# Kernel optimization log

Hardware: AMD Instinct MI355X
Metric: run time of the kernel (lower is better)

The kernel has to match this reference:

```python
import jax, jax.numpy as jnp
import numpy as np

TOPK = 8

def setup_inputs() -> dict:
    key = jax.random.key(0)
    k1, k2, k3, k4, k5 = jax.random.split(key, 5)
    B, S, D, E = 8, 2048, 4096, 64
    scale = 1.0 / np.sqrt(D)
    x = jax.random.normal(k1, (B, S, D), dtype=jnp.float32)
    Wr = jax.random.uniform(k2, (D, E), dtype=jnp.float32, minval=-scale, maxval=scale)
    br = jax.random.uniform(k3, (E,), dtype=jnp.float32, minval=-scale, maxval=scale)
    Wn = jax.random.uniform(k4, (D, E), dtype=jnp.float32, minval=-scale, maxval=scale)
    bn = jax.random.uniform(k5, (E,), dtype=jnp.float32, minval=-scale, maxval=scale)
    return {"x": x, "Wr": Wr, "br": br, "Wn": Wn, "bn": bn}

def reference(x, Wr, br, Wn, bn):
    B, S, D = x.shape
    E = Wr.shape[1]
    logits = jnp.einsum('bsd,de->bse', x, Wr) + br          # [B,S,E]
    # NOTE: original module computes noisy_logits = logits + randn*noisy_vec but
    # then takes topk/softmax on the CLEAN logits, so the noise branch is dead code.
    noisy_vec = jnp.einsum('bsd,de->bse', x, Wn) + bn       # computed, unused (faithful)
    del noisy_vec
    topk_vals, topk_idx = jax.lax.top_k(logits, TOPK)       # [B,S,K]
    T = B * S
    flat_vals = topk_vals.reshape(T, TOPK)
    flat_idx = topk_idx.reshape(T, TOPK)
    sparse = jnp.full((T, E), -jnp.inf, dtype=logits.dtype)
    sparse = sparse.at[jnp.arange(T)[:, None], flat_idx].set(flat_vals)
    router_scores = jax.nn.softmax(sparse, axis=-1).reshape(B, S, E)
    return router_scores, topk_idx
```

## Files before the change

### kernel.cpp

```cpp
#include <hip/hip_runtime.h>
#include <math.h>

#define DDIM 4096
#define EDIM 64
#define NROWS 16384
#define MBLK 32
#define KT 64
#define NKT (DDIM / KT)
#define TOPK_K 8
#define DIGIT_BIAS 0x00808080

typedef int i32x4 __attribute__((ext_vector_type(4)));

__device__ __forceinline__ int digits_of(float f) {
  int v = __float2int_rn(f);
  return (v + DIGIT_BIAS) ^ DIGIT_BIAS;
}

__device__ __forceinline__ unsigned perm_b32(unsigned a, unsigned b, unsigned sel) {
#if __has_builtin(__builtin_amdgcn_perm)
  return __builtin_amdgcn_perm(a, b, sel);
#else
  union { unsigned u[2]; unsigned char c[8]; } s; s.u[0] = b; s.u[1] = a;
  unsigned r = 0;
  for (int i = 0; i < 4; ++i) r |= (unsigned)s.c[(sel >> (8*i)) & 7] << (8*i);
  return r;
#endif
}

__global__ __launch_bounds__(256) void wr_convert(const float* __restrict__ Wr,
                                                  char* __restrict__ wl8) {
  int t = blockIdx.x * 256 + threadIdx.x;
  int e = t & 63, k16 = t >> 6;
  int kt64 = k16 >> 2, kgg = k16 & 3, nf = e >> 4, col = e & 15;
  int D[16];
  #pragma unroll
  for (int j = 0; j < 16; ++j)
    D[j] = digits_of(Wr[(size_t)(k16 * 16 + j) * EDIM + e] * 68719476736.0f);
  #pragma unroll
  for (int pl = 0; pl < 4; ++pl) {
    unsigned wv[4];
    #pragma unroll
    for (int g = 0; g < 4; ++g)
      wv[g] = ((unsigned)((D[4*g+0] >> (8*pl)) & 255))
            | ((unsigned)((D[4*g+1] >> (8*pl)) & 255) << 8)
            | ((unsigned)((D[4*g+2] >> (8*pl)) & 255) << 16)
            | ((unsigned)((D[4*g+3] >> (8*pl)) & 255) << 24);
    i32x4 val = {(int)wv[0], (int)wv[1], (int)wv[2], (int)wv[3]};
    *(i32x4*)(wl8 + (size_t)pl * 262144 + (size_t)(kt64 * 4 + nf) * 1024
              + (size_t)(kgg * 16 + col) * 16) = val;
  }
}

__global__ __launch_bounds__(512, 4) void router_fused(
    const float* __restrict__ x, const char* __restrict__ wl8,
    const float* __restrict__ br,
    float* __restrict__ out_scores, float* __restrict__ out_idx) {
  __shared__ __align__(16) char smem[2][24576];

  const int tid  = threadIdx.x;
  const int lane = tid & 63;
  const int w    = tid >> 6;
  const int mw   = w >> 2;
  const int nw   = w & 3;
  const int kg   = lane >> 4;
  const int row0 = blockIdx.x * MBLK;
  const int row_l = mw * 16 + (lane & 15);
  const int srow = w * 4 + (lane >> 4);
  const float bias = br[nw * 16 + (lane & 15)];

  i32x4 acc[5] = {};

  auto stage = [&](int t, int b) {
    #pragma unroll
    for (int i = 0; i < 2; ++i) {
      int c = w * 2 + i;
      int plane = c >> 2, nf = c & 3;
      const char* src = wl8 + (size_t)plane * 262144 +
                        (size_t)(t * 4 + nf) * 1024 + (size_t)lane * 16;
      __builtin_amdgcn_global_load_lds(
          (const __attribute__((address_space(1))) unsigned int*)(const void*)src,
          (__attribute__((address_space(3))) unsigned int*)(void*)&smem[b][c * 1024],
          16, 0, 0);
    }
    {
      int cc = lane & 15;
      const float* src = x + (size_t)(row0 + srow) * DDIM + t * KT
                           + ((cc ^ (srow & 7)) << 2);
      __builtin_amdgcn_global_load_lds(
          (const __attribute__((address_space(1))) unsigned int*)(const void*)src,
          (__attribute__((address_space(3))) unsigned int*)(void*)
              &smem[b][16384 + w * 1024],
          16, 0, 0);
    }
  };

  auto compute = [&](int b) {
    const char* Wb = smem[b];
    const char* Xb = smem[b] + 16384;
    float4 xv[4];
    #pragma unroll
    for (int c = 0; c < 4; ++c) {
      int chunk = (kg * 4 + c) ^ (row_l & 7);
      xv[c] = *(const float4*)(Xb + row_l * 256 + chunk * 16);
    }
    i32x4 a0, a1, a2, a3;
    #pragma unroll
    for (int g = 0; g < 4; ++g) {
      float4 v = xv[g];
      unsigned f0 = (unsigned)digits_of(v.x * 33554432.0f);
      unsigned f1 = (unsigned)digits_of(v.y * 33554432.0f);
      unsigned f2 = (unsigned)digits_of(v.z * 33554432.0f);
      unsigned f3 = (unsigned)digits_of(v.w * 33554432.0f);
      unsigned zl01 = perm_b32(f1, f0, 0x05010400u);
      unsigned zh01 = perm_b32(f1, f0, 0x07030602u);
      unsigned zl23 = perm_b32(f3, f2, 0x05010400u);
      unsigned zh23 = perm_b32(f3, f2, 0x07030602u);
      a0[g] = (int)perm_b32(zl23, zl01, 0x05040100u);
      a1[g] = (int)perm_b32(zl23, zl01, 0x07060302u);
      a2[g] = (int)perm_b32(zh23, zh01, 0x05040100u);
      a3[g] = (int)perm_b32(zh23, zh01, 0x07060302u);
    }
    i32x4 b0 = *(const i32x4*)(Wb + (0 * 4 + nw) * 1024 + lane * 16);
    i32x4 b1 = *(const i32x4*)(Wb + (1 * 4 + nw) * 1024 + lane * 16);
    i32x4 b2 = *(const i32x4*)(Wb + (2 * 4 + nw) * 1024 + lane * 16);
    i32x4 b3 = *(const i32x4*)(Wb + (3 * 4 + nw) * 1024 + lane * 16);

    acc[0] = __builtin_amdgcn_mfma_i32_16x16x64_i8(a3, b3, acc[0], 0, 0, 0);
    acc[1] = __builtin_amdgcn_mfma_i32_16x16x64_i8(a3, b2, acc[1], 0, 0, 0);
    acc[1] = __builtin_amdgcn_mfma_i32_16x16x64_i8(a2, b3, acc[1], 0, 0, 0);
    acc[2] = __builtin_amdgcn_mfma_i32_16x16x64_i8(a3, b1, acc[2], 0, 0, 0);
    acc[2] = __builtin_amdgcn_mfma_i32_16x16x64_i8(a2, b2, acc[2], 0, 0, 0);
    acc[2] = __builtin_amdgcn_mfma_i32_16x16x64_i8(a1, b3, acc[2], 0, 0, 0);
    acc[3] = __builtin_amdgcn_mfma_i32_16x16x64_i8(a3, b0, acc[3], 0, 0, 0);
    acc[3] = __builtin_amdgcn_mfma_i32_16x16x64_i8(a2, b1, acc[3], 0, 0, 0);
    acc[3] = __builtin_amdgcn_mfma_i32_16x16x64_i8(a1, b2, acc[3], 0, 0, 0);
    acc[3] = __builtin_amdgcn_mfma_i32_16x16x64_i8(a0, b3, acc[3], 0, 0, 0);
    acc[4] = __builtin_amdgcn_mfma_i32_16x16x64_i8(a2, b0, acc[4], 0, 0, 0);
    acc[4] = __builtin_amdgcn_mfma_i32_16x16x64_i8(a1, b1, acc[4], 0, 0, 0);
    acc[4] = __builtin_amdgcn_mfma_i32_16x16x64_i8(a0, b2, acc[4], 0, 0, 0);
  };

  stage(0, 0);
  __syncthreads();
  for (int t = 0; t < NKT; ++t) {
    if (t + 1 < NKT) stage(t + 1, (t + 1) & 1);
    compute(t & 1);
    __syncthreads();
  }

  double* ls = (double*)smem;
  {
    int cc = nw * 16 + (lane & 15);
    #pragma unroll
    for (int j = 0; j < 4; ++j) {
      int r = mw * 16 + (lane >> 4) * 4 + j;
      double lg = (double)acc[0][j] * 0x1p-13 + (double)acc[1][j] * 0x1p-21
                + (double)acc[2][j] * 0x1p-29 + (double)acc[3][j] * 0x1p-37
                + (double)acc[4][j] * 0x1p-45 + (double)bias;
      ls[r * 64 + cc] = lg;
    }
  }
  __syncthreads();

  for (int rr = 0; rr < 4; ++rr) {
    int r = w * 4 + rr;
    double v0 = ls[r * 64 + lane];
    double cur = v0;
    bool sel  = false;
    int myidx = 0;
    double maxv = 0.0;
    #pragma unroll
    for (int k = 0; k < TOPK_K; ++k) {
      double bv = cur;
      int    bi = lane;
      #pragma unroll
      for (int off = 32; off; off >>= 1) {
        double ov = __shfl_xor(bv, off);
        int    oi = __shfl_xor(bi, off);
        if (ov > bv || (ov == bv && oi < bi)) { bv = ov; bi = oi; }
      }
      if (k == 0) maxv = bv;
      if (lane == k) myidx = bi;
      if (lane == bi) { cur = -__builtin_inf(); sel = true; }
    }
    float pv = sel ? expf((float)(v0 - maxv)) : 0.f;
    float ssum = pv;
    #pragma unroll
    for (int off = 32; off; off >>= 1) ssum += __shfl_xor(ssum, off);

    size_t rg = (size_t)row0 + r;
    out_scores[rg * 64 + lane] = pv / ssum;
    if (lane < TOPK_K) out_idx[rg * 8 + lane] = (float)myidx;
  }
}

extern "C" void kernel_launch(void* const* d_in, const int* in_sizes, int n_in,
                              void* d_out, int out_size, void* d_ws, size_t ws_size,
                              hipStream_t stream) {
  const float* x  = (const float*)d_in[0];
  const float* Wr = (const float*)d_in[1];
  const float* br = (const float*)d_in[2];

  char* wl8 = (char*)d_ws;
  float* out_scores = (float*)d_out;
  float* out_idx    = out_scores + (size_t)NROWS * EDIM;

  wr_convert<<<64, 256, 0, stream>>>(Wr, wl8);
  router_fused<<<NROWS / MBLK, 512, 0, stream>>>(x, wl8, br, out_scores, out_idx);
}
```

Baseline: 127.3 us.

## Replace LDS-staged main loop with direct register double-buffered global loads

```diff
diff --git a/kernel.cpp b/kernel.cpp
--- a/kernel.cpp
+++ b/kernel.cpp
@@ -5,15 +5,18 @@
 #define EDIM 64
 #define NROWS 16384
 #define MBLK 32
-#define KT 64
-#define NKT (DDIM / KT)
+#define NKT 64
 #define TOPK_K 8
 #define DIGIT_BIAS 0x00808080
 
 typedef int i32x4 __attribute__((ext_vector_type(4)));
 
-__device__ __forceinline__ int digits_of(float f) {
+__device__ __forceinline__ int digits_rn(float f) {
   int v = __float2int_rn(f);
+  return (v + DIGIT_BIAS) ^ DIGIT_BIAS;
+}
+__device__ __forceinline__ int digits_tz(float f) {
+  int v = (int)f;
   return (v + DIGIT_BIAS) ^ DIGIT_BIAS;
 }
 
@@ -36,7 +39,7 @@
   int D[16];
   #pragma unroll
   for (int j = 0; j < 16; ++j)
-    D[j] = digits_of(Wr[(size_t)(k16 * 16 + j) * EDIM + e] * 68719476736.0f);
+    D[j] = digits_rn(Wr[(size_t)(k16 * 16 + j) * EDIM + e] * 68719476736.0f);
   #pragma unroll
   for (int pl = 0; pl < 4; ++pl) {
     unsigned wv[4];
@@ -56,7 +59,7 @@
     const float* __restrict__ x, const char* __restrict__ wl8,
     const float* __restrict__ br,
     float* __restrict__ out_scores, float* __restrict__ out_idx) {
-  __shared__ __align__(16) char smem[2][24576];
+  __shared__ double ls[MBLK * EDIM];
 
   const int tid  = threadIdx.x;
   const int lane = tid & 63;
@@ -66,90 +69,69 @@
   const int kg   = lane >> 4;
   const int row0 = blockIdx.x * MBLK;
   const int row_l = mw * 16 + (lane & 15);
-  const int srow = w * 4 + (lane >> 4);
   const float bias = br[nw * 16 + (lane & 15)];
 
+  const char* xr = (const char*)x + ((size_t)(row0 + row_l)) * (DDIM * 4) + kg * 64;
+  const char* wr = wl8 + (size_t)nw * 1024 + (size_t)lane * 16;
+
   i32x4 acc[5] = {};
+  float4 X0[4], X1[4];
+  i32x4  B0[4], B1[4];
+  i32x4  A[4];
 
-  auto stage = [&](int t, int b) {
+  auto loadX = [&](int t, float4 (&X)[4]) {
+    const char* p = xr + t * 256;
     #pragma unroll
-    for (int i = 0; i < 2; ++i) {
-      int c = w * 2 + i;
-      int plane = c >> 2, nf = c & 3;
-      const char* src = wl8 + (size_t)plane * 262144 +
-                        (size_t)(t * 4 + nf) * 1024 + (size_t)lane * 16;
-      __builtin_amdgcn_global_load_lds(
-          (const __attribute__((address_space(1))) unsigned int*)(const void*)src,
-          (__attribute__((address_space(3))) unsigned int*)(void*)&smem[b][c * 1024],
-          16, 0, 0);
-    }
-    {
-      int cc = lane & 15;
-      const float* src = x + (size_t)(row0 + srow) * DDIM + t * KT
-                           + ((cc ^ (srow & 7)) << 2);
-      __builtin_amdgcn_global_load_lds(
-          (const __attribute__((address_space(1))) unsigned int*)(const void*)src,
-          (__attribute__((address_space(3))) unsigned int*)(void*)
-              &smem[b][16384 + w * 1024],
-          16, 0, 0);
-    }
+    for (int c = 0; c < 4; ++c) X[c] = *(const float4*)(p + c * 16);
+  };
+  auto loadB = [&](int t, i32x4 (&B)[4]) {
+    const char* p = wr + (size_t)t * 4096;
+    #pragma unroll
+    for (int pl = 0; pl < 4; ++pl)
+      B[pl] = *(const i32x4*)(p + (size_t)pl * 262144);
+  };
+  auto cvtg = [&](const float4& v, int g) {
+    unsigned f0 = (unsigned)digits_tz(v.x * 33554432.0f);
+    unsigned f1 = (unsigned)digits_tz(v.y * 33554432.0f);
+    unsigned f2 = (unsigned)digits_tz(v.z * 33554432.0f);
+    unsigned f3 = (unsigned)digits_tz(v.w * 33554432.0f);
+    unsigned zl01 = perm_b32(f1, f0, 0x05010400u);
+    unsigned zh01 = perm_b32(f1, f0, 0x07030602u);
+    unsigned zl23 = perm_b32(f3, f2, 0x05010400u);
+    unsigned zh23 = perm_b32(f3, f2, 0x07030602u);
+    A[0][g] = (int)perm_b32(zl23, zl01, 0x05040100u);
+    A[1][g] = (int)perm_b32(zl23, zl01, 0x07060302u);
+    A[2][g] = (int)perm_b32(zh23, zh01, 0x05040100u);
+    A[3][g] = (int)perm_b32(zh23, zh01, 0x07060302u);
+  };
+  auto mfmaAll = [&](i32x4 (&b)[4]) {
+    acc[0] = __builtin_amdgcn_mfma_i32_16x16x64_i8(A[3], b[3], acc[0], 0, 0, 0);
+    acc[1] = __builtin_amdgcn_mfma_i32_16x16x64_i8(A[3], b[2], acc[1], 0, 0, 0);
+    acc[2] = __builtin_amdgcn_mfma_i32_16x16x64_i8(A[3], b[1], acc[2], 0, 0, 0);
+    acc[3] = __builtin_amdgcn_mfma_i32_16x16x64_i8(A[3], b[0], acc[3], 0, 0, 0);
+    acc[4] = __builtin_amdgcn_mfma_i32_16x16x64_i8(A[2], b[0], acc[4], 0, 0, 0);
+    acc[1] = __builtin_amdgcn_mfma_i32_16x16x64_i8(A[2], b[3], acc[1], 0, 0, 0);
+    acc[2] = __builtin_amdgcn_mfma_i32_16x16x64_i8(A[2], b[2], acc[2], 0, 0, 0);
+    acc[3] = __builtin_amdgcn_mfma_i32_16x16x64_i8(A[2], b[1], acc[3], 0, 0, 0);
+    acc[4] = __builtin_amdgcn_mfma_i32_16x16x64_i8(A[1], b[1], acc[4], 0, 0, 0);
+    acc[2] = __builtin_amdgcn_mfma_i32_16x16x64_i8(A[1], b[3], acc[2], 0, 0, 0);
+    acc[3] = __builtin_amdgcn_mfma_i32_16x16x64_i8(A[1], b[2], acc[3], 0, 0, 0);
+    acc[4] = __builtin_amdgcn_mfma_i32_16x16x64_i8(A[0], b[2], acc[4], 0, 0, 0);
+    acc[3] = __builtin_amdgcn_mfma_i32_16x16x64_i8(A[0], b[3], acc[3], 0, 0, 0);
   };
 
-  auto compute = [&](int b) {
-    const char* Wb = smem[b];
-    const char* Xb = smem[b] + 16384;
-    float4 xv[4];
-    #pragma unroll
-    for (int c = 0; c < 4; ++c) {
-      int chunk = (kg * 4 + c) ^ (row_l & 7);
-      xv[c] = *(const float4*)(Xb + row_l * 256 + chunk * 16);
-    }
-    i32x4 a0, a1, a2, a3;
-    #pragma unroll
-    for (int g = 0; g < 4; ++g) {
-      float4 v = xv[g];
-      unsigned f0 = (unsigned)digits_of(v.x * 33554432.0f);
-      unsigned f1 = (unsigned)digits_of(v.y * 33554432.0f);
-      unsigned f2 = (unsigned)digits_of(v.z * 33554432.0f);
-      unsigned f3 = (unsigned)digits_of(v.w * 33554432.0f);
-      unsigned zl01 = perm_b32(f1, f0, 0x05010400u);
-      unsigned zh01 = perm_b32(f1, f0, 0x07030602u);
-      unsigned zl23 = perm_b32(f3, f2, 0x05010400u);
-      unsigned zh23 = perm_b32(f3, f2, 0x07030602u);
-      a0[g] = (int)perm_b32(zl23, zl01, 0x05040100u);
-      a1[g] = (int)perm_b32(zl23, zl01, 0x07060302u);
-      a2[g] = (int)perm_b32(zh23, zh01, 0x05040100u);
-      a3[g] = (int)perm_b32(zh23, zh01, 0x07060302u);
-    }
-    i32x4 b0 = *(const i32x4*)(Wb + (0 * 4 + nw) * 1024 + lane * 16);
-    i32x4 b1 = *(const i32x4*)(Wb + (1 * 4 + nw) * 1024 + lane * 16);
-    i32x4 b2 = *(const i32x4*)(Wb + (2 * 4 + nw) * 1024 + lane * 16);
-    i32x4 b3 = *(const i32x4*)(Wb + (3 * 4 + nw) * 1024 + lane * 16);
+  loadB(0, B0); loadX(0, X0);
+  loadB(1, B1); loadX(1, X1);
 
-    acc[0] = __builtin_amdgcn_mfma_i32_16x16x64_i8(a3, b3, acc[0], 0, 0, 0);
-    acc[1] = __builtin_amdgcn_mfma_i32_16x16x64_i8(a3, b2, acc[1], 0, 0, 0);
-    acc[1] = __builtin_amdgcn_mfma_i32_16x16x64_i8(a2, b3, acc[1], 0, 0, 0);
-    acc[2] = __builtin_amdgcn_mfma_i32_16x16x64_i8(a3, b1, acc[2], 0, 0, 0);
-    acc[2] = __builtin_amdgcn_mfma_i32_16x16x64_i8(a2, b2, acc[2], 0, 0, 0);
-    acc[2] = __builtin_amdgcn_mfma_i32_16x16x64_i8(a1, b3, acc[2], 0, 0, 0);
-    acc[3] = __builtin_amdgcn_mfma_i32_16x16x64_i8(a3, b0, acc[3], 0, 0, 0);
-    acc[3] = __builtin_amdgcn_mfma_i32_16x16x64_i8(a2, b1, acc[3], 0, 0, 0);
-    acc[3] = __builtin_amdgcn_mfma_i32_16x16x64_i8(a1, b2, acc[3], 0, 0, 0);
-    acc[3] = __builtin_amdgcn_mfma_i32_16x16x64_i8(a0, b3, acc[3], 0, 0, 0);
-    acc[4] = __builtin_amdgcn_mfma_i32_16x16x64_i8(a2, b0, acc[4], 0, 0, 0);
-    acc[4] = __builtin_amdgcn_mfma_i32_16x16x64_i8(a1, b1, acc[4], 0, 0, 0);
-    acc[4] = __builtin_amdgcn_mfma_i32_16x16x64_i8(a0, b2, acc[4], 0, 0, 0);
-  };
-
-  stage(0, 0);
-  __syncthreads();
-  for (int t = 0; t < NKT; ++t) {
-    if (t + 1 < NKT) stage(t + 1, (t + 1) & 1);
-    compute(t & 1);
-    __syncthreads();
+  for (int t = 0; t < NKT; t += 2) {
+    cvtg(X0[0], 0); cvtg(X0[1], 1); cvtg(X0[2], 2); cvtg(X0[3], 3);
+    mfmaAll(B0);
+    if (t + 2 < NKT) { loadB(t + 2, B0); loadX(t + 2, X0); }
+    cvtg(X1[0], 0); cvtg(X1[1], 1); cvtg(X1[2], 2); cvtg(X1[3], 3);
+    mfmaAll(B1);
+    if (t + 3 < NKT) { loadB(t + 3, B1); loadX(t + 3, X1); }
   }
 
-  double* ls = (double*)smem;
   {
     int cc = nw * 16 + (lane & 15);
     #pragma unroll
```

After: 188.0 us. 47.6% more time.
